# Kernel tuning notes

Measured on AMD Instinct MI355X. Metric: run time of the kernel, lower is better.

## Reference

```python
import jax, jax.numpy as jnp
import numpy as np

N = 100000
E = 3200000
F_IN = 256
HID = 128


def _dconv_k1(x_cat, w, b):
    # torch_geometric_temporal DConv with K=1:
    # H = X @ W[0,0] + X @ W[1,0] + b   (no graph propagation for K=1)
    return x_cat @ (w[0, 0] + w[1, 0]) + b


def _dcrnn_cell(x, h, wz, bz, wr, br, wh, bh):
    xh = jnp.concatenate([x, h], axis=1)
    z = jax.nn.sigmoid(_dconv_k1(xh, wz, bz))
    r = jax.nn.sigmoid(_dconv_k1(xh, wr, br))
    xrh = jnp.concatenate([x, r * h], axis=1)
    h_tilde = jnp.tanh(_dconv_k1(xrh, wh, bh))
    return z * h + (1.0 - z) * h_tilde


def setup_inputs() -> dict:
    key = jax.random.key(0)
    ks = jax.random.split(key, 16)

    def gw(k, shape):
        fan_in = shape[-2]
        return jax.random.normal(k, shape, dtype=jnp.float32) / np.sqrt(fan_in)

    inp = {
        "x": jax.random.normal(ks[0], (N, F_IN), dtype=jnp.float32),
        "edge_index": jax.random.randint(ks[1], (2, E), 0, N, dtype=jnp.int64 if jax.config.jax_enable_x64 else jnp.int32),
        "edge_weight": jax.random.uniform(ks[2], (E,), dtype=jnp.float32),
        "w_z1": gw(ks[3], (2, 1, F_IN + HID, HID)), "b_z1": jnp.zeros((HID,), jnp.float32),
        "w_r1": gw(ks[4], (2, 1, F_IN + HID, HID)), "b_r1": jnp.zeros((HID,), jnp.float32),
        "w_h1": gw(ks[5], (2, 1, F_IN + HID, HID)), "b_h1": jnp.zeros((HID,), jnp.float32),
        "w_z2": gw(ks[6], (2, 1, HID + HID // 2, HID // 2)), "b_z2": jnp.zeros((HID // 2,), jnp.float32),
        "w_r2": gw(ks[7], (2, 1, HID + HID // 2, HID // 2)), "b_r2": jnp.zeros((HID // 2,), jnp.float32),
        "w_h2": gw(ks[8], (2, 1, HID + HID // 2, HID // 2)), "b_h2": jnp.zeros((HID // 2,), jnp.float32),
        "w_lin1": gw(ks[9], (HID // 2, 16)), "b_lin1": jnp.zeros((16,), jnp.float32),
        "w_lin2": gw(ks[10], (16, 1)), "b_lin2": jnp.zeros((1,), jnp.float32),
    }
    return inp


def reference(x, edge_index, edge_weight,
              w_z1, b_z1, w_r1, b_r1, w_h1, b_h1,
              w_z2, b_z2, w_r2, b_r2, w_h2, b_h2,
              w_lin1, b_lin1, w_lin2, b_lin2):
    # edge_index / edge_weight are unused in the K=1 DConv math (faithful to tgt source).
    h0 = jnp.zeros((x.shape[0], w_z1.shape[-1]), x.dtype)
    h = _dcrnn_cell(x, h0, w_z1, b_z1, w_r1, b_r1, w_h1, b_h1)
    h = jax.nn.relu(h)
    h0b = jnp.zeros((x.shape[0], w_z2.shape[-1]), x.dtype)
    h = _dcrnn_cell(h, h0b, w_z2, b_z2, w_r2, b_r2, w_h2, b_h2)
    h = jax.nn.relu(h)
    # Dropout(0.2) is identity at inference
    h = jax.nn.relu(h @ w_lin1 + b_lin1)
    return h @ w_lin2 + b_lin2
```

## Files before the change

kernel.cpp:

```cpp
#include <hip/hip_runtime.h>

typedef _Float16 f16;
typedef _Float16 f16x8 __attribute__((ext_vector_type(8)));
typedef float    f32x4 __attribute__((ext_vector_type(4)));

#define N_ROWS 100000
#define RT 782
#define PAD_ROWS (RT * 128)
#define LS 72

#define W1T_OFF 0
#define W1T_BYTES (256 * 256 * 2)
#define W2T_OFF (W1T_OFF + W1T_BYTES)
#define W2T_BYTES (128 * 128 * 2)
#define H1_OFF (W2T_OFF + W2T_BYTES)
#define H1_BYTES (PAD_ROWS * 128 * 2)
#define H2_OFF (H1_OFF + H1_BYTES)

__global__ void prep_w1(const float* __restrict__ wz, const float* __restrict__ wh,
                        f16* __restrict__ W1T) {
    int idx = blockIdx.x * 256 + threadIdx.x;
    int k = idx >> 8;
    int c = idx & 255;
    const float* w = (c < 128) ? wz : wh;
    int cc = c & 127;
    float v = w[k * 128 + cc] + w[384 * 128 + k * 128 + cc];
    W1T[c * 256 + k] = (f16)v;
}

__global__ void prep_w2(const float* __restrict__ wz, const float* __restrict__ wh,
                        f16* __restrict__ W2T) {
    int idx = blockIdx.x * 256 + threadIdx.x;
    int k = idx >> 7;
    int c = idx & 127;
    const float* w = (c < 64) ? wz : wh;
    int cc = c & 63;
    float v = w[k * 64 + cc] + w[192 * 64 + k * 64 + cc];
    W2T[c * 128 + k] = (f16)v;
}

__global__ __launch_bounds__(256) void k1_layer1(const float* __restrict__ x,
                                                 const f16* __restrict__ W1T,
                                                 const float* __restrict__ bz,
                                                 const float* __restrict__ bh,
                                                 f16* __restrict__ h1) {
    __shared__ __align__(16) f16 Xs[128 * LS];
    __shared__ __align__(16) f16 Ws[128 * LS];

    const int tid  = threadIdx.x;
    const int r0   = blockIdx.x * 128;
    const int jt   = blockIdx.y;
    const int lane = tid & 63, wave = tid >> 6;
    const int ln   = lane & 15, quad = lane >> 4;
    const int rh   = wave >> 1, jh = wave & 1;

    float4 xa[4], xb[4];
    f16x8  wv[4];

#define K1_LOAD(KB)                                                              \
    _Pragma("unroll")                                                            \
    for (int it2 = 0; it2 < 4; ++it2) {                                          \
        const int idx = (it2 << 8) + tid;                                        \
        const int row = idx >> 3, cc = idx & 7;                                  \
        const int gr  = (r0 + row < N_ROWS) ? (r0 + row) : (N_ROWS - 1);         \
        const float* xp = x + (size_t)gr * 256 + (KB) + (cc << 3);               \
        xa[it2] = *(const float4*)xp;                                            \
        xb[it2] = *(const float4*)(xp + 4);                                      \
        const int grow = (jt << 6) + row + ((row < 64) ? 0 : 64);                \
        wv[it2] = *(const f16x8*)(W1T + ((size_t)grow << 8) + (KB) + (cc << 3)); \
    }

    K1_LOAD(0)

    f32x4 acc[4][2][2];
#pragma unroll
    for (int a = 0; a < 4; ++a)
#pragma unroll
        for (int b = 0; b < 2; ++b)
#pragma unroll
            for (int g = 0; g < 2; ++g) acc[a][b][g] = (f32x4){0.f, 0.f, 0.f, 0.f};

    for (int kb = 0; kb < 256; kb += 64) {
#pragma unroll
        for (int it2 = 0; it2 < 4; ++it2) {
            const int idx = (it2 << 8) + tid;
            const int row = idx >> 3, cc = idx & 7;
            f16x8 p = {(f16)xa[it2].x, (f16)xa[it2].y, (f16)xa[it2].z, (f16)xa[it2].w,
                       (f16)xb[it2].x, (f16)xb[it2].y, (f16)xb[it2].z, (f16)xb[it2].w};
            *(f16x8*)&Xs[row * LS + (cc << 3)] = p;
            *(f16x8*)&Ws[row * LS + (cc << 3)] = wv[it2];
        }
        __syncthreads();
        if (kb < 192) { K1_LOAD(kb + 64) }

#pragma unroll
        for (int kc = 0; kc < 2; ++kc) {
            f16x8 af[4], bzf[2], bhf[2];
#pragma unroll
            for (int rb = 0; rb < 4; ++rb)
                af[rb] = *(const f16x8*)&Xs[(64 * rh + 16 * rb + ln) * LS + kc * 32 + quad * 8];
#pragma unroll
            for (int cb = 0; cb < 2; ++cb) {
                bzf[cb] = *(const f16x8*)&Ws[(32 * jh + 16 * cb + ln) * LS + kc * 32 + quad * 8];
                bhf[cb] = *(const f16x8*)&Ws[(64 + 32 * jh + 16 * cb + ln) * LS + kc * 32 + quad * 8];
            }
#pragma unroll
            for (int rb = 0; rb < 4; ++rb)
#pragma unroll
                for (int cb = 0; cb < 2; ++cb) {
                    acc[rb][cb][0] = __builtin_amdgcn_mfma_f32_16x16x32_f16(af[rb], bzf[cb], acc[rb][cb][0], 0, 0, 0);
                    acc[rb][cb][1] = __builtin_amdgcn_mfma_f32_16x16x32_f16(af[rb], bhf[cb], acc[rb][cb][1], 0, 0, 0);
                }
        }
        __syncthreads();
    }
#undef K1_LOAD

#pragma unroll
    for (int cb = 0; cb < 2; ++cb) {
        const int jg = (jt << 6) + 32 * jh + 16 * cb + ln;
        const float bzv = bz[jg];
        const float bhv = bh[jg];
#pragma unroll
        for (int rb = 0; rb < 4; ++rb) {
            const int rbase = r0 + 64 * rh + 16 * rb + 4 * quad;
#pragma unroll
            for (int i = 0; i < 4; ++i) {
                float zp = acc[rb][cb][0][i] + bzv;
                float hp = acc[rb][cb][1][i] + bhv;
                float ex = __expf(2.0f * hp);
                float th = 1.0f - 2.0f / (ex + 1.0f);
                float sg = 1.0f / (1.0f + __expf(zp));
                float g = fmaxf(th * sg, 0.0f);
                h1[(size_t)(rbase + i) * 128 + jg] = (f16)g;
            }
        }
    }
}

__global__ __launch_bounds__(256) void k2_layer2(const f16* __restrict__ h1,
                                                 const f16* __restrict__ W2T,
                                                 const float* __restrict__ bz,
                                                 const float* __restrict__ bh,
                                                 f16* __restrict__ h2) {
    __shared__ __align__(16) f16 Xs[128 * LS];
    __shared__ __align__(16) f16 Ws[128 * LS];

    const int tid  = threadIdx.x;
    const int r0   = blockIdx.x * 128;
    const int lane = tid & 63, wave = tid >> 6;
    const int ln   = lane & 15, quad = lane >> 4;
    const int rh   = wave >> 1, jh = wave & 1;

    f16x8 xv[4], wv[4];

#define K2_LOAD(KB)                                                               \
    _Pragma("unroll")                                                             \
    for (int it2 = 0; it2 < 4; ++it2) {                                           \
        const int idx = (it2 << 8) + tid;                                         \
        const int row = idx >> 3, cc = idx & 7;                                   \
        xv[it2] = *(const f16x8*)(h1 + ((size_t)(r0 + row) << 7) + (KB) + (cc << 3)); \
        wv[it2] = *(const f16x8*)(W2T + ((size_t)row << 7) + (KB) + (cc << 3));   \
    }

    K2_LOAD(0)

    f32x4 acc[4][2][2];
#pragma unroll
    for (int a = 0; a < 4; ++a)
#pragma unroll
        for (int b = 0; b < 2; ++b)
#pragma unroll
            for (int g = 0; g < 2; ++g) acc[a][b][g] = (f32x4){0.f, 0.f, 0.f, 0.f};

    for (int kb = 0; kb < 128; kb += 64) {
#pragma unroll
        for (int it2 = 0; it2 < 4; ++it2) {
            const int idx = (it2 << 8) + tid;
            const int row = idx >> 3, cc = idx & 7;
            *(f16x8*)&Xs[row * LS + (cc << 3)] = xv[it2];
            *(f16x8*)&Ws[row * LS + (cc << 3)] = wv[it2];
        }
        __syncthreads();
        if (kb == 0) { K2_LOAD(64) }

#pragma unroll
        for (int kc = 0; kc < 2; ++kc) {
            f16x8 af[4], bzf[2], bhf[2];
#pragma unroll
            for (int rb = 0; rb < 4; ++rb)
                af[rb] = *(const f16x8*)&Xs[(64 * rh + 16 * rb + ln) * LS + kc * 32 + quad * 8];
#pragma unroll
            for (int cb = 0; cb < 2; ++cb) {
                bzf[cb] = *(const f16x8*)&Ws[(32 * jh + 16 * cb + ln) * LS + kc * 32 + quad * 8];
                bhf[cb] = *(const f16x8*)&Ws[(64 + 32 * jh + 16 * cb + ln) * LS + kc * 32 + quad * 8];
            }
#pragma unroll
            for (int rb = 0; rb < 4; ++rb)
#pragma unroll
                for (int cb = 0; cb < 2; ++cb) {
                    acc[rb][cb][0] = __builtin_amdgcn_mfma_f32_16x16x32_f16(af[rb], bzf[cb], acc[rb][cb][0], 0, 0, 0);
                    acc[rb][cb][1] = __builtin_amdgcn_mfma_f32_16x16x32_f16(af[rb], bhf[cb], acc[rb][cb][1], 0, 0, 0);
                }
        }
        __syncthreads();
    }
#undef K2_LOAD

#pragma unroll
    for (int cb = 0; cb < 2; ++cb) {
        const int j = 32 * jh + 16 * cb + ln;
        const float bzv = bz[j];
        const float bhv = bh[j];
#pragma unroll
        for (int rb = 0; rb < 4; ++rb) {
            const int rbase = r0 + 64 * rh + 16 * rb + 4 * quad;
#pragma unroll
            for (int i = 0; i < 4; ++i) {
                float zp = acc[rb][cb][0][i] + bzv;
                float hp = acc[rb][cb][1][i] + bhv;
                float ex = __expf(2.0f * hp);
                float th = 1.0f - 2.0f / (ex + 1.0f);
                float sg = 1.0f / (1.0f + __expf(zp));
                float g = fmaxf(th * sg, 0.0f);
                h2[(size_t)(rbase + i) * 64 + j] = (f16)g;
            }
        }
    }
}

__global__ __launch_bounds__(256) void k3_lin(const f16* __restrict__ h2,
                                              const float* __restrict__ wl1,
                                              const float* __restrict__ bl1,
                                              const float* __restrict__ wl2,
                                              const float* __restrict__ bl2,
                                              float* __restrict__ out) {
    const int row = blockIdx.x * 256 + threadIdx.x;
    if (row >= N_ROWS) return;
    const f16x8* hp = (const f16x8*)(h2 + (size_t)row * 64);
    float xf[64];
#pragma unroll
    for (int i = 0; i < 8; ++i) {
        f16x8 v = hp[i];
#pragma unroll
        for (int j = 0; j < 8; ++j) xf[i * 8 + j] = (float)v[j];
    }
    float acc[16];
#pragma unroll
    for (int j = 0; j < 16; ++j) acc[j] = bl1[j];
#pragma unroll
    for (int k = 0; k < 64; ++k) {
#pragma unroll
        for (int j = 0; j < 16; ++j) acc[j] = fmaf(xf[k], wl1[k * 16 + j], acc[j]);
    }
    float o = bl2[0];
#pragma unroll
    for (int j = 0; j < 16; ++j) o = fmaf(fmaxf(acc[j], 0.0f), wl2[j], o);
    out[row] = o;
}

extern "C" void kernel_launch(void* const* d_in, const int* in_sizes, int n_in,
                              void* d_out, int out_size, void* d_ws, size_t ws_size,
                              hipStream_t stream) {
    const float* x   = (const float*)d_in[0];
    const float* wz1 = (const float*)d_in[3];
    const float* bz1 = (const float*)d_in[4];
    const float* wh1 = (const float*)d_in[7];
    const float* bh1 = (const float*)d_in[8];
    const float* wz2 = (const float*)d_in[9];
    const float* bz2 = (const float*)d_in[10];
    const float* wh2 = (const float*)d_in[13];
    const float* bh2 = (const float*)d_in[14];
    const float* wl1 = (const float*)d_in[15];
    const float* bl1 = (const float*)d_in[16];
    const float* wl2 = (const float*)d_in[17];
    const float* bl2 = (const float*)d_in[18];

    char* ws = (char*)d_ws;
    f16* W1T = (f16*)(ws + W1T_OFF);
    f16* W2T = (f16*)(ws + W2T_OFF);
    f16* h1  = (f16*)(ws + H1_OFF);
    f16* h2  = (f16*)(ws + H2_OFF);
    float* out = (float*)d_out;

    prep_w1<<<256, 256, 0, stream>>>(wz1, wh1, W1T);
    prep_w2<<<64, 256, 0, stream>>>(wz2, wh2, W2T);
    k1_layer1<<<dim3(RT, 2), 256, 0, stream>>>(x, W1T, bz1, bh1, h1);
    k2_layer2<<<RT, 256, 0, stream>>>(h1, W2T, bz2, bh2, h2);
    k3_lin<<<391, 256, 0, stream>>>(h2, wl1, bl1, wl2, bl2, out);
}
```

Baseline: 256.3 us.

## Fuse both DCRNN layers and linear head into one kernel with LDS-resident activations

Merges layer1, layer2 and the linear head into a single kernel. Each 128-row block now computes all 256 layer-1 output columns, keeps h1 and h2 in shared memory, and computes the final projection with MFMA plus lane shuffles. Weights are loaded straight into LDS with global_load_lds using an XOR swizzle. This removes the global round-trips for h1 and h2, two launches, and reading x twice across column tiles. In exchange the block uses more LDS and registers (launch bounds of 2 blocks per CU), which lowers occupancy.

```diff
diff --git a/kernel.cpp b/kernel.cpp
--- a/kernel.cpp
+++ b/kernel.cpp
@@ -1,21 +1,31 @@
 #include <hip/hip_runtime.h>
 
 typedef _Float16 f16;
+typedef _Float16 f16x4 __attribute__((ext_vector_type(4)));
 typedef _Float16 f16x8 __attribute__((ext_vector_type(8)));
 typedef float    f32x4 __attribute__((ext_vector_type(4)));
 
 #define N_ROWS 100000
 #define RT 782
-#define PAD_ROWS (RT * 128)
-#define LS 72
 
 #define W1T_OFF 0
 #define W1T_BYTES (256 * 256 * 2)
-#define W2T_OFF (W1T_OFF + W1T_BYTES)
-#define W2T_BYTES (128 * 128 * 2)
-#define H1_OFF (W2T_OFF + W2T_BYTES)
-#define H1_BYTES (PAD_ROWS * 128 * 2)
-#define H2_OFF (H1_OFF + H1_BYTES)
+#define W2T_OFF W1T_BYTES
+
+#define A_XS 0
+#define A_WS 18432
+#define A_H1 0
+#define A_W2 36864
+#define A_H2 0
+#define ARENA_BYTES 69632
+#define LSX 72
+#define LSH1 136
+#define LSH2 72
+
+__device__ __forceinline__ void glds16(const void* g, void* l) {
+    __builtin_amdgcn_global_load_lds((const __attribute__((address_space(1))) void*)g,
+                                     (__attribute__((address_space(3))) void*)l, 16, 0, 0);
+}
 
 __global__ void prep_w1(const float* __restrict__ wz, const float* __restrict__ wh,
                         f16* __restrict__ W1T) {
@@ -39,46 +49,46 @@
     W2T[c * 128 + k] = (f16)v;
 }
 
-__global__ __launch_bounds__(256) void k1_layer1(const float* __restrict__ x,
-                                                 const f16* __restrict__ W1T,
-                                                 const float* __restrict__ bz,
-                                                 const float* __restrict__ bh,
-                                                 f16* __restrict__ h1) {
-    __shared__ __align__(16) f16 Xs[128 * LS];
-    __shared__ __align__(16) f16 Ws[128 * LS];
-
-    const int tid  = threadIdx.x;
-    const int r0   = blockIdx.x * 128;
-    const int jt   = blockIdx.y;
-    const int lane = tid & 63, wave = tid >> 6;
-    const int ln   = lane & 15, quad = lane >> 4;
-    const int rh   = wave >> 1, jh = wave & 1;
+__global__ __launch_bounds__(256, 2) void fused(
+    const float* __restrict__ x,
+    const f16* __restrict__ W1T, const f16* __restrict__ W2T,
+    const float* __restrict__ bz1, const float* __restrict__ bh1,
+    const float* __restrict__ bz2, const float* __restrict__ bh2,
+    const float* __restrict__ wl1, const float* __restrict__ bl1,
+    const float* __restrict__ wl2, const float* __restrict__ bl2,
+    float* __restrict__ out)
+{
+    __shared__ __align__(16) char arena[ARENA_BYTES];
+    const int tid = threadIdx.x, lane = tid & 63, wave = tid >> 6;
+    const int ln = lane & 15, quad = lane >> 4;
+    const int rh = wave >> 1, jh = wave & 1;
+    const int r0 = blockIdx.x * 128;
+
+    f16* Xs = (f16*)(arena + A_XS);
+    f16* Ws = (f16*)(arena + A_WS);
 
     float4 xa[4], xb[4];
-    f16x8  wv[4];
-
-#define K1_LOAD(KB)                                                              \
+
+#define X_LOAD(KB)                                                               \
     _Pragma("unroll")                                                            \
     for (int it2 = 0; it2 < 4; ++it2) {                                          \
         const int idx = (it2 << 8) + tid;                                        \
         const int row = idx >> 3, cc = idx & 7;                                  \
-        const int gr  = (r0 + row < N_ROWS) ? (r0 + row) : (N_ROWS - 1);         \
+        const int gr = (r0 + row < N_ROWS) ? (r0 + row) : (N_ROWS - 1);          \
         const float* xp = x + (size_t)gr * 256 + (KB) + (cc << 3);               \
         xa[it2] = *(const float4*)xp;                                            \
         xb[it2] = *(const float4*)(xp + 4);                                      \
-        const int grow = (jt << 6) + row + ((row < 64) ? 0 : 64);                \
-        wv[it2] = *(const f16x8*)(W1T + ((size_t)grow << 8) + (KB) + (cc << 3)); \
-    }
-
-    K1_LOAD(0)
-
-    f32x4 acc[4][2][2];
-#pragma unroll
-    for (int a = 0; a < 4; ++a)
-#pragma unroll
-        for (int b = 0; b < 2; ++b)
-#pragma unroll
-            for (int g = 0; g < 2; ++g) acc[a][b][g] = (f32x4){0.f, 0.f, 0.f, 0.f};
+    }
+
+    X_LOAD(0)
+
+    f32x4 acc[8][4];
+#pragma unroll
+    for (int a = 0; a < 8; ++a)
+#pragma unroll
+        for (int b = 0; b < 4; ++b) acc[a][b] = (f32x4){0.f, 0.f, 0.f, 0.f};
+
+    const int wrloc = lane >> 3, wslot = lane & 7;
 
     for (int kb = 0; kb < 256; kb += 64) {
 #pragma unroll
@@ -87,176 +97,158 @@
             const int row = idx >> 3, cc = idx & 7;
             f16x8 p = {(f16)xa[it2].x, (f16)xa[it2].y, (f16)xa[it2].z, (f16)xa[it2].w,
                        (f16)xb[it2].x, (f16)xb[it2].y, (f16)xb[it2].z, (f16)xb[it2].w};
-            *(f16x8*)&Xs[row * LS + (cc << 3)] = p;
-            *(f16x8*)&Ws[row * LS + (cc << 3)] = wv[it2];
+            *(f16x8*)&Xs[row * LSX + (cc << 3)] = p;
+        }
+#pragma unroll
+        for (int c = 0; c < 8; ++c) {
+            const int h = wave * 8 + c;
+            const int col = h * 8 + wrloc;
+            glds16(W1T + (size_t)col * 256 + kb + ((wslot ^ (col & 7)) << 3),
+                   Ws + h * 512);
         }
         __syncthreads();
-        if (kb < 192) { K1_LOAD(kb + 64) }
+        if (kb < 192) { X_LOAD(kb + 64) }
 
 #pragma unroll
         for (int kc = 0; kc < 2; ++kc) {
-            f16x8 af[4], bzf[2], bhf[2];
-#pragma unroll
-            for (int rb = 0; rb < 4; ++rb)
-                af[rb] = *(const f16x8*)&Xs[(64 * rh + 16 * rb + ln) * LS + kc * 32 + quad * 8];
-#pragma unroll
-            for (int cb = 0; cb < 2; ++cb) {
-                bzf[cb] = *(const f16x8*)&Ws[(32 * jh + 16 * cb + ln) * LS + kc * 32 + quad * 8];
-                bhf[cb] = *(const f16x8*)&Ws[(64 + 32 * jh + 16 * cb + ln) * LS + kc * 32 + quad * 8];
-            }
-#pragma unroll
-            for (int rb = 0; rb < 4; ++rb)
-#pragma unroll
-                for (int cb = 0; cb < 2; ++cb) {
-                    acc[rb][cb][0] = __builtin_amdgcn_mfma_f32_16x16x32_f16(af[rb], bzf[cb], acc[rb][cb][0], 0, 0, 0);
-                    acc[rb][cb][1] = __builtin_amdgcn_mfma_f32_16x16x32_f16(af[rb], bhf[cb], acc[rb][cb][1], 0, 0, 0);
-                }
+            f16x8 bf[4];
+#pragma unroll
+            for (int nt = 0; nt < 4; ++nt)
+                bf[nt] = *(const f16x8*)&Xs[((rh << 6) + (nt << 4) + ln) * LSX + kc * 32 + quad * 8];
+            const int sw = ((kc * 4 + quad) ^ (ln & 7)) << 3;
+#pragma unroll
+            for (int mt = 0; mt < 8; ++mt) {
+                const int col = ((mt & 3) << 4) + (jh << 6) + ((mt >> 2) << 7) + ln;
+                f16x8 af = *(const f16x8*)&Ws[col * 64 + sw];
+#pragma unroll
+                for (int nt = 0; nt < 4; ++nt)
+                    acc[mt][nt] = __builtin_amdgcn_mfma_f32_16x16x32_f16(af, bf[nt], acc[mt][nt], 0, 0, 0);
+            }
         }
         __syncthreads();
     }
-#undef K1_LOAD
-
-#pragma unroll
-    for (int cb = 0; cb < 2; ++cb) {
-        const int jg = (jt << 6) + 32 * jh + 16 * cb + ln;
-        const float bzv = bz[jg];
-        const float bhv = bh[jg];
-#pragma unroll
-        for (int rb = 0; rb < 4; ++rb) {
-            const int rbase = r0 + 64 * rh + 16 * rb + 4 * quad;
+#undef X_LOAD
+
+    f16* h1s = (f16*)(arena + A_H1);
+#pragma unroll
+    for (int mtp = 0; mtp < 4; ++mtp) {
+        const int jg0 = (jh << 6) + (mtp << 4) + (quad << 2);
+        const float4 zb4 = *(const float4*)(bz1 + jg0);
+        const float4 hb4 = *(const float4*)(bh1 + jg0);
+        const float zbv[4] = {zb4.x, zb4.y, zb4.z, zb4.w};
+        const float hbv[4] = {hb4.x, hb4.y, hb4.z, hb4.w};
+#pragma unroll
+        for (int nt = 0; nt < 4; ++nt) {
+            const int row = (rh << 6) + (nt << 4) + ln;
+            f16x4 pk;
 #pragma unroll
             for (int i = 0; i < 4; ++i) {
-                float zp = acc[rb][cb][0][i] + bzv;
-                float hp = acc[rb][cb][1][i] + bhv;
+                float zp = acc[mtp][nt][i] + zbv[i];
+                float hp = acc[mtp + 4][nt][i] + hbv[i];
                 float ex = __expf(2.0f * hp);
                 float th = 1.0f - 2.0f / (ex + 1.0f);
                 float sg = 1.0f / (1.0f + __expf(zp));
-                float g = fmaxf(th * sg, 0.0f);
-                h1[(size_t)(rbase + i) * 128 + jg] = (f16)g;
-            }
-        }
-    }
-}
-
-__global__ __launch_bounds__(256) void k2_layer2(const f16* __restrict__ h1,
-                                                 const f16* __restrict__ W2T,
-                                                 const float* __restrict__ bz,
-                                                 const float* __restrict__ bh,
-                                                 f16* __restrict__ h2) {
-    __shared__ __align__(16) f16 Xs[128 * LS];
-    __shared__ __align__(16) f16 Ws[128 * LS];
-
-    const int tid  = threadIdx.x;
-    const int r0   = blockIdx.x * 128;
-    const int lane = tid & 63, wave = tid >> 6;
-    const int ln   = lane & 15, quad = lane >> 4;
-    const int rh   = wave >> 1, jh = wave & 1;
-
-    f16x8 xv[4], wv[4];
-
-#define K2_LOAD(KB)                                                               \
-    _Pragma("unroll")                                                             \
-    for (int it2 = 0; it2 < 4; ++it2) {                                           \
-        const int idx = (it2 << 8) + tid;                                         \
-        const int row = idx >> 3, cc = idx & 7;                                   \
-        xv[it2] = *(const f16x8*)(h1 + ((size_t)(r0 + row) << 7) + (KB) + (cc << 3)); \
-        wv[it2] = *(const f16x8*)(W2T + ((size_t)row << 7) + (KB) + (cc << 3));   \
-    }
-
-    K2_LOAD(0)
-
-    f32x4 acc[4][2][2];
+                pk[i] = (f16)fmaxf(th * sg, 0.0f);
+            }
+            *(f16x4*)&h1s[row * LSH1 + jg0] = pk;
+        }
+    }
+
+    f16* W2s = (f16*)(arena + A_W2);
+    {
+        const int rloc = lane >> 4, s = lane & 15;
+#pragma unroll
+        for (int c = 0; c < 8; ++c) {
+            const int h = wave * 8 + c;
+            const int col = h * 4 + rloc;
+            glds16(W2T + (size_t)col * 128 + ((s ^ (col & 15)) << 3), W2s + h * 512);
+        }
+    }
+    __syncthreads();
+
+    f32x4 acc2[4][4];
 #pragma unroll
     for (int a = 0; a < 4; ++a)
 #pragma unroll
-        for (int b = 0; b < 2; ++b)
-#pragma unroll
-            for (int g = 0; g < 2; ++g) acc[a][b][g] = (f32x4){0.f, 0.f, 0.f, 0.f};
-
-    for (int kb = 0; kb < 128; kb += 64) {
-#pragma unroll
-        for (int it2 = 0; it2 < 4; ++it2) {
-            const int idx = (it2 << 8) + tid;
-            const int row = idx >> 3, cc = idx & 7;
-            *(f16x8*)&Xs[row * LS + (cc << 3)] = xv[it2];
-            *(f16x8*)&Ws[row * LS + (cc << 3)] = wv[it2];
-        }
-        __syncthreads();
-        if (kb == 0) { K2_LOAD(64) }
-
-#pragma unroll
-        for (int kc = 0; kc < 2; ++kc) {
-            f16x8 af[4], bzf[2], bhf[2];
-#pragma unroll
-            for (int rb = 0; rb < 4; ++rb)
-                af[rb] = *(const f16x8*)&Xs[(64 * rh + 16 * rb + ln) * LS + kc * 32 + quad * 8];
-#pragma unroll
-            for (int cb = 0; cb < 2; ++cb) {
-                bzf[cb] = *(const f16x8*)&Ws[(32 * jh + 16 * cb + ln) * LS + kc * 32 + quad * 8];
-                bhf[cb] = *(const f16x8*)&Ws[(64 + 32 * jh + 16 * cb + ln) * LS + kc * 32 + quad * 8];
-            }
-#pragma unroll
-            for (int rb = 0; rb < 4; ++rb)
-#pragma unroll
-                for (int cb = 0; cb < 2; ++cb) {
-                    acc[rb][cb][0] = __builtin_amdgcn_mfma_f32_16x16x32_f16(af[rb], bzf[cb], acc[rb][cb][0], 0, 0, 0);
-                    acc[rb][cb][1] = __builtin_amdgcn_mfma_f32_16x16x32_f16(af[rb], bhf[cb], acc[rb][cb][1], 0, 0, 0);
-                }
-        }
-        __syncthreads();
-    }
-#undef K2_LOAD
-
-#pragma unroll
-    for (int cb = 0; cb < 2; ++cb) {
-        const int j = 32 * jh + 16 * cb + ln;
-        const float bzv = bz[j];
-        const float bhv = bh[j];
-#pragma unroll
-        for (int rb = 0; rb < 4; ++rb) {
-            const int rbase = r0 + 64 * rh + 16 * rb + 4 * quad;
+        for (int b = 0; b < 4; ++b) acc2[a][b] = (f32x4){0.f, 0.f, 0.f, 0.f};
+
+#pragma unroll
+    for (int kc = 0; kc < 4; ++kc) {
+        f16x8 bf[4];
+#pragma unroll
+        for (int nt = 0; nt < 4; ++nt)
+            bf[nt] = *(const f16x8*)&h1s[((rh << 6) + (nt << 4) + ln) * LSH1 + kc * 32 + quad * 8];
+        const int sw = ((kc * 4 + quad) ^ ln) << 3;
+#pragma unroll
+        for (int mt = 0; mt < 4; ++mt) {
+            const int col = ((mt & 1) << 4) + (jh << 5) + ((mt >> 1) << 6) + ln;
+            f16x8 af = *(const f16x8*)&W2s[col * 128 + sw];
+#pragma unroll
+            for (int nt = 0; nt < 4; ++nt)
+                acc2[mt][nt] = __builtin_amdgcn_mfma_f32_16x16x32_f16(af, bf[nt], acc2[mt][nt], 0, 0, 0);
+        }
+    }
+    __syncthreads();
+
+    f16* h2s = (f16*)(arena + A_H2);
+#pragma unroll
+    for (int mtp = 0; mtp < 2; ++mtp) {
+        const int jg0 = (jh << 5) + (mtp << 4) + (quad << 2);
+        const float4 zb4 = *(const float4*)(bz2 + jg0);
+        const float4 hb4 = *(const float4*)(bh2 + jg0);
+        const float zbv[4] = {zb4.x, zb4.y, zb4.z, zb4.w};
+        const float hbv[4] = {hb4.x, hb4.y, hb4.z, hb4.w};
+#pragma unroll
+        for (int nt = 0; nt < 4; ++nt) {
+            const int row = (rh << 6) + (nt << 4) + ln;
+            f16x4 pk;
 #pragma unroll
             for (int i = 0; i < 4; ++i) {
-                float zp = acc[rb][cb][0][i] + bzv;
-                float hp = acc[rb][cb][1][i] + bhv;
+                float zp = acc2[mtp][nt][i] + zbv[i];
+                float hp = acc2[mtp + 2][nt][i] + hbv[i];
                 float ex = __expf(2.0f * hp);
                 float th = 1.0f - 2.0f / (ex + 1.0f);
                 float sg = 1.0f / (1.0f + __expf(zp));
-                float g = fmaxf(th * sg, 0.0f);
-                h2[(size_t)(rbase + i) * 64 + j] = (f16)g;
-            }
-        }
-    }
-}
-
-__global__ __launch_bounds__(256) void k3_lin(const f16* __restrict__ h2,
-                                              const float* __restrict__ wl1,
-                                              const float* __restrict__ bl1,
-                                              const float* __restrict__ wl2,
-                                              const float* __restrict__ bl2,
-                                              float* __restrict__ out) {
-    const int row = blockIdx.x * 256 + threadIdx.x;
-    if (row >= N_ROWS) return;
-    const f16x8* hp = (const f16x8*)(h2 + (size_t)row * 64);
-    float xf[64];
-#pragma unroll
-    for (int i = 0; i < 8; ++i) {
-        f16x8 v = hp[i];
-#pragma unroll
-        for (int j = 0; j < 8; ++j) xf[i * 8 + j] = (float)v[j];
-    }
-    float acc[16];
-#pragma unroll
-    for (int j = 0; j < 16; ++j) acc[j] = bl1[j];
-#pragma unroll
-    for (int k = 0; k < 64; ++k) {
-#pragma unroll
-        for (int j = 0; j < 16; ++j) acc[j] = fmaf(xf[k], wl1[k * 16 + j], acc[j]);
-    }
-    float o = bl2[0];
-#pragma unroll
-    for (int j = 0; j < 16; ++j) o = fmaf(fmaxf(acc[j], 0.0f), wl2[j], o);
-    out[row] = o;
+                pk[i] = (f16)fmaxf(th * sg, 0.0f);
+            }
+            *(f16x4*)&h2s[row * LSH2 + jg0] = pk;
+        }
+    }
+    __syncthreads();
+
+    const float blv  = bl1[ln];
+    const float wlv  = wl2[ln];
+    const float bl2v = bl2[0];
+    f16x8 bfr[2];
+#pragma unroll
+    for (int kc = 0; kc < 2; ++kc)
+#pragma unroll
+        for (int j = 0; j < 8; ++j)
+            bfr[kc][j] = (f16)wl1[(kc * 32 + quad * 8 + j) * 16 + ln];
+
+    f32x4 acc3[2] = {(f32x4){0.f, 0.f, 0.f, 0.f}, (f32x4){0.f, 0.f, 0.f, 0.f}};
+#pragma unroll
+    for (int t2 = 0; t2 < 2; ++t2)
+#pragma unroll
+        for (int kc = 0; kc < 2; ++kc) {
+            f16x8 af = *(const f16x8*)&h2s[((wave << 5) + (t2 << 4) + ln) * LSH2 + kc * 32 + quad * 8];
+            acc3[t2] = __builtin_amdgcn_mfma_f32_16x16x32_f16(af, bfr[kc], acc3[t2], 0, 0, 0);
+        }
+
+#pragma unroll
+    for (int t2 = 0; t2 < 2; ++t2)
+#pragma unroll
+        for (int i = 0; i < 4; ++i) {
+            float v = fmaxf(acc3[t2][i] + blv, 0.0f) * wlv;
+            v += __shfl_xor(v, 1);
+            v += __shfl_xor(v, 2);
+            v += __shfl_xor(v, 4);
+            v += __shfl_xor(v, 8);
+            if (ln == 0) {
+                const int row = r0 + (wave << 5) + (t2 << 4) + (quad << 2) + i;
+                if (row < N_ROWS) out[row] = v + bl2v;
+            }
+        }
 }
 
 extern "C" void kernel_launch(void* const* d_in, const int* in_sizes, int n_in,
@@ -279,13 +271,10 @@
     char* ws = (char*)d_ws;
     f16* W1T = (f16*)(ws + W1T_OFF);
     f16* W2T = (f16*)(ws + W2T_OFF);
-    f16* h1  = (f16*)(ws + H1_OFF);
-    f16* h2  = (f16*)(ws + H2_OFF);
     float* out = (float*)d_out;
 
     prep_w1<<<256, 256, 0, stream>>>(wz1, wh1, W1T);
     prep_w2<<<64, 256, 0, stream>>>(wz2, wh2, W2T);
-    k1_layer1<<<dim3(RT, 2), 256, 0, stream>>>(x, W1T, bz1, bh1, h1);
-    k2_layer2<<<RT, 256, 0, stream>>>(h1, W2T, bz2, bh2, h2);
-    k3_lin<<<391, 256, 0, stream>>>(h2, wl1, bl1, wl2, bl2, out);
-}
+    fused<<<RT, 256, 0, stream>>>(x, W1T, W2T, bz1, bh1, bz2, bh2,
+                                  wl1, bl1, wl2, bl2, out);
+}
```

New measurement: 246.7 us. 1.04x faster.
